# Kernel tuning notes

Hardware: AMD Instinct MI355X
Metric: run time of the kernel (lower is better)

Reference implementation:

```python
import jax, jax.numpy as jnp
import numpy as np

N_NODES = 20000
N_EDGES = 160000
N_GRAPHS = 100
IN_CH = 64
EDGE_DIM = 8
NEG_SLOPE = 0.2


def _gatv2(x, edge_index, edge_attr, Wl, Wr, We, att, b, heads, ch, n_nodes):
    # GATv2Conv: e_ij = att . leaky_relu(Wl x_j + Wr x_i [+ We e_ij]), softmax over dst i,
    # out_i = sum_j alpha_ij * (Wl x_j), concat heads, + bias.
    src, dst = edge_index[0], edge_index[1]
    xl = (x @ Wl).reshape(-1, heads, ch)  # [N,H,C] source-side transform
    xr = (x @ Wr).reshape(-1, heads, ch)  # [N,H,C] target-side transform
    m = xl[src] + xr[dst]                 # [E,H,C]
    if edge_attr is not None:
        m = m + (edge_attr @ We).reshape(-1, heads, ch)
    m = jax.nn.leaky_relu(m, NEG_SLOPE)
    logit = jnp.einsum('ehc,hc->eh', m, att)                     # [E,H]
    mx = jax.ops.segment_max(logit, dst, num_segments=n_nodes)   # [N,H]
    ex = jnp.exp(logit - mx[dst])
    den = jax.ops.segment_sum(ex, dst, num_segments=n_nodes)     # [N,H]
    alpha = ex / (den[dst] + 1e-16)                              # [E,H]
    out = jax.ops.segment_sum(alpha[:, :, None] * xl[src], dst, num_segments=n_nodes)
    return out.reshape(-1, heads * ch) + b


def setup_inputs() -> dict:
    key = jax.random.key(0)
    ks = jax.random.split(key, 24)
    def rn(k, shape, fan_in):
        return jax.random.normal(k, shape, dtype=jnp.float32) / np.sqrt(fan_in)
    inp = {}
    inp['x'] = jax.random.normal(ks[0], (N_NODES, IN_CH), dtype=jnp.float32)
    inp['edge_attr'] = jax.random.uniform(ks[1], (N_EDGES, EDGE_DIM), dtype=jnp.float32)
    inp['Wl1'] = rn(ks[2], (IN_CH, 1024), IN_CH)
    inp['Wr1'] = rn(ks[3], (IN_CH, 1024), IN_CH)
    inp['We1'] = rn(ks[4], (EDGE_DIM, 1024), EDGE_DIM)
    inp['att1'] = rn(ks[5], (4, 256), 256)
    inp['b1'] = jnp.zeros((1024,), jnp.float32)
    inp['Wl2'] = rn(ks[6], (1024, 256), 1024)
    inp['Wr2'] = rn(ks[7], (1024, 256), 1024)
    inp['We2'] = rn(ks[8], (EDGE_DIM, 256), EDGE_DIM)
    inp['att2'] = rn(ks[9], (4, 64), 64)
    inp['b2'] = jnp.zeros((256,), jnp.float32)
    inp['Wlp'] = rn(ks[10], (256, 384), 256)
    inp['Wrp'] = rn(ks[11], (256, 384), 256)
    inp['attp'] = rn(ks[12], (6, 64), 64)
    inp['bp'] = jnp.zeros((384,), jnp.float32)
    inp['Wfc1'] = rn(ks[13], (384, 64), 384)
    inp['bfc1'] = jnp.zeros((64,), jnp.float32)
    inp['Wfc2'] = rn(ks[14], (64, 1), 64)
    inp['bfc2'] = jnp.zeros((1,), jnp.float32)
    inp['edge_index'] = jax.random.randint(ks[15], (2, N_EDGES), 0, N_NODES, dtype=jnp.int32)
    inp['edge_index_master'] = jax.random.randint(ks[16], (2, N_EDGES), 0, N_NODES, dtype=jnp.int32)
    inp['n_nodes'] = jnp.full((N_GRAPHS,), N_NODES // N_GRAPHS, dtype=jnp.int32)
    return inp


def reference(x, edge_attr, Wl1, Wr1, We1, att1, b1, Wl2, Wr2, We2, att2, b2,
              Wlp, Wrp, attp, bp, Wfc1, bfc1, Wfc2, bfc2,
              edge_index, edge_index_master, n_nodes):
    h = _gatv2(x, edge_index, edge_attr, Wl1, Wr1, We1, att1, b1, 4, 256, N_NODES)
    h = jax.nn.relu(h)
    h = _gatv2(h, edge_index, edge_attr, Wl2, Wr2, We2, att2, b2, 4, 64, N_NODES)
    h = jax.nn.relu(h)
    h = _gatv2(h, edge_index_master, None, Wlp, Wrp, None, attp, bp, 6, 64, N_NODES)
    last_idx = jnp.cumsum(n_nodes) - 1          # master node = last node of each graph
    master = h[last_idx]                        # [G,384] (dropout p=0 -> identity)
    z = jax.nn.relu(master @ Wfc1 + bfc1)
    return z @ Wfc2 + bfc2                      # [G,1]
```

## Files before the change

kernel.cpp:

```cpp
#include <hip/hip_runtime.h>
#include <hip/hip_bf16.h>

#define DIV_UP(a,b) (((a)+(b)-1)/(b))

typedef __attribute__((ext_vector_type(8))) short short8;
typedef __attribute__((ext_vector_type(4))) float floatx4;

static __device__ __forceinline__ unsigned short f2bf(float v) {
    unsigned u = __builtin_bit_cast(unsigned, v);
    u += 0x7fffu + ((u >> 16) & 1u);
    return (unsigned short)(u >> 16);
}
static __device__ __forceinline__ float bflo(unsigned v) {
    return __builtin_bit_cast(float, v << 16);
}
static __device__ __forceinline__ float bfhi(unsigned v) {
    return __builtin_bit_cast(float, v & 0xffff0000u);
}

template <int CPL>
static __device__ __forceinline__ void load_bf16v(const unsigned short* p, float* d) {
    if constexpr (CPL == 8) {
        uint4 v = *(const uint4*)p;
        d[0] = bflo(v.x); d[1] = bfhi(v.x);
        d[2] = bflo(v.y); d[3] = bfhi(v.y);
        d[4] = bflo(v.z); d[5] = bfhi(v.z);
        d[6] = bflo(v.w); d[7] = bfhi(v.w);
    } else if constexpr (CPL == 4) {
        uint2 v = *(const uint2*)p;
        d[0] = bflo(v.x); d[1] = bfhi(v.x);
        d[2] = bflo(v.y); d[3] = bfhi(v.y);
    } else if constexpr (CPL == 2) {
        unsigned v = *(const unsigned*)p;
        d[0] = bflo(v); d[1] = bfhi(v);
    } else {
        d[0] = bflo(*p);
    }
}

template <int CPL>
static __device__ __forceinline__ void store_bf16v(unsigned short* p, const float* s) {
    unsigned short tmp[CPL];
#pragma unroll
    for (int c = 0; c < CPL; ++c) tmp[c] = f2bf(s[c]);
    if constexpr (CPL == 8) *(uint4*)p = *(uint4*)tmp;
    else if constexpr (CPL == 4) *(ushort4*)p = *(ushort4*)tmp;
    else if constexpr (CPL == 2) *(ushort2*)p = *(ushort2*)tmp;
    else p[0] = tmp[0];
}

template <int CTRL>
static __device__ __forceinline__ float dpp_mv(float x) {
    int r = __builtin_amdgcn_update_dpp(0, __builtin_bit_cast(int, x), CTRL, 0xF, 0xF, false);
    return __builtin_bit_cast(float, r);
}
template <int G>
static __device__ __forceinline__ float group_reduce(float x) {
    x += dpp_mv<0xB1>(x);
    x += dpp_mv<0x4E>(x);
    x += dpp_mv<0x124>(x);
    x += dpp_mv<0x128>(x);
    if constexpr (G >= 32) x += __shfl_xor(x, 16, 64);
    if constexpr (G >= 64) x += __shfl_xor(x, 32, 64);
    return x;
}

static __device__ __forceinline__ void tr_pair(const float* Wa, const float* Wb, int K, int Nn,
                                               unsigned short* Wt, int i) {
    int tot = K * Nn;
    const float* W = (i < tot) ? Wa : Wb;
    unsigned short* dst = Wt + ((i < tot) ? 0 : (size_t)Nn * K);
    int ii = (i < tot) ? i : i - tot;
    int k = ii % K, n = ii / K;
    dst[(size_t)n * K + k] = f2bf(W[(size_t)k * Nn + n]);
}

__global__ void prep_all(const float* __restrict__ x,
                         const float* __restrict__ Wl1, const float* __restrict__ Wr1,
                         const float* __restrict__ Wl2, const float* __restrict__ Wr2,
                         const float* __restrict__ Wlp, const float* __restrict__ Wrp,
                         unsigned short* __restrict__ xbf,
                         unsigned short* __restrict__ wt1, unsigned short* __restrict__ wt2,
                         unsigned short* __restrict__ wt3, int N) {
    const int S1 = 2 * 64 * 1024, S2 = 2 * 1024 * 256, S3 = 2 * 256 * 384;
    int id = blockIdx.x * blockDim.x + threadIdx.x;
    if (id < S1) tr_pair(Wl1, Wr1, 64, 1024, wt1, id);
    else if (id < S1 + S2) tr_pair(Wl2, Wr2, 1024, 256, wt2, id - S1);
    else if (id < S1 + S2 + S3) tr_pair(Wlp, Wrp, 256, 384, wt3, id - S1 - S2);
    else {
        int i = id - S1 - S2 - S3;
        if (i < N * 64) xbf[i] = f2bf(x[i]);
    }
}

__global__ __launch_bounds__(256) void gemm_mfma(
    const unsigned short* __restrict__ A, const unsigned short* __restrict__ Bt,
    unsigned short* __restrict__ C, int M, int Ntot, int K) {
    constexpr int LDA = 40;
    __shared__ unsigned short As[128 * LDA];
    __shared__ unsigned short Bs[128 * LDA];
    const int tid = threadIdx.x;
    const int m0 = blockIdx.y * 128, n0 = blockIdx.x * 128;
    const int wave = tid >> 6, lane = tid & 63;
    const int wm = (wave >> 1) * 64, wn = (wave & 1) * 64;
    const int r15 = lane & 15, quad = lane >> 4;
    const int sr = tid >> 1, skc = tid & 1;
    floatx4 acc[4][4];
#pragma unroll
    for (int i = 0; i < 4; ++i)
#pragma unroll
        for (int j = 0; j < 4; ++j) acc[i][j] = (floatx4)0.f;

    for (int k0 = 0; k0 < K; k0 += 32) {
        uint4 a0 = make_uint4(0, 0, 0, 0), a1 = make_uint4(0, 0, 0, 0);
        int am = m0 + sr;
        if (am < M) {
            const unsigned short* ap = A + (size_t)am * K + k0 + skc * 16;
            a0 = *(const uint4*)ap;
            a1 = *(const uint4*)(ap + 8);
        }
        const unsigned short* bp = Bt + (size_t)(n0 + sr) * K + k0 + skc * 16;
        uint4 b0 = *(const uint4*)bp;
        uint4 b1 = *(const uint4*)(bp + 8);
        *(uint4*)(&As[sr * LDA + skc * 16]) = a0;
        *(uint4*)(&As[sr * LDA + skc * 16 + 8]) = a1;
        *(uint4*)(&Bs[sr * LDA + skc * 16]) = b0;
        *(uint4*)(&Bs[sr * LDA + skc * 16 + 8]) = b1;
        __syncthreads();
        short8 af[4], bfr[4];
#pragma unroll
        for (int i = 0; i < 4; ++i)
            af[i] = *(const short8*)(&As[(wm + i * 16 + r15) * LDA + quad * 8]);
#pragma unroll
        for (int j = 0; j < 4; ++j)
            bfr[j] = *(const short8*)(&Bs[(wn + j * 16 + r15) * LDA + quad * 8]);
#pragma unroll
        for (int i = 0; i < 4; ++i)
#pragma unroll
            for (int j = 0; j < 4; ++j)
                acc[i][j] = __builtin_amdgcn_mfma_f32_16x16x32_bf16(af[i], bfr[j], acc[i][j], 0, 0, 0);
        __syncthreads();
    }
#pragma unroll
    for (int i = 0; i < 4; ++i)
#pragma unroll
        for (int j = 0; j < 4; ++j)
#pragma unroll
            for (int r = 0; r < 4; ++r) {
                int m = m0 + wm + i * 16 + quad * 4 + r;
                int n = n0 + wn + j * 16 + r15;
                if (m < M) C[(size_t)m * Ntot + n] = f2bf(acc[i][j][r]);
            }
}

__global__ void count2_kernel(const int* __restrict__ dst0, const int* __restrict__ dst1,
                              int E, int N, int* __restrict__ cnt) {
    int e = blockIdx.x * blockDim.x + threadIdx.x;
    if (e < E) atomicAdd(&cnt[dst0[e]], 1);
    else if (e < 2 * E) atomicAdd(&cnt[N + dst1[e - E]], 1);
}

__global__ __launch_bounds__(1024) void scan_kernel(const int* __restrict__ cnt_all, int N,
                                                    int* __restrict__ off_all, int* __restrict__ cur_all) {
    const int* cnt = cnt_all + blockIdx.x * N;
    int* off = off_all + blockIdx.x * (N + 1);
    int* cur = cur_all + blockIdx.x * N;
    __shared__ int part[1024];
    int t = threadIdx.x;
    int per = (N + 1023) >> 10;
    int base = t * per;
    int s = 0;
    for (int i = 0; i < per; ++i) { int idx = base + i; if (idx < N) s += cnt[idx]; }
    part[t] = s;
    __syncthreads();
    for (int d2 = 1; d2 < 1024; d2 <<= 1) {
        int v = (t >= d2) ? part[t - d2] : 0;
        __syncthreads();
        part[t] += v;
        __syncthreads();
    }
    int pre = (t == 0) ? 0 : part[t - 1];
    for (int i = 0; i < per; ++i) {
        int idx = base + i;
        if (idx < N) { off[idx] = pre; cur[idx] = pre; pre += cnt[idx]; }
    }
    if (t == 1023) off[N] = part[1023];
}

__global__ void fill2_kernel(const int* __restrict__ src0, const int* __restrict__ dst0,
                             const int* __restrict__ src1, const int* __restrict__ dst1,
                             int E, int N, int* __restrict__ cur, int2* __restrict__ edges) {
    int e = blockIdx.x * blockDim.x + threadIdx.x;
    if (e < E) {
        int p = atomicAdd(&cur[dst0[e]], 1);
        edges[p] = make_int2(src0[e], e);
    } else if (e < 2 * E) {
        int i = e - E;
        int p = atomicAdd(&cur[N + dst1[i]], 1);
        edges[E + p] = make_int2(src1[i], i);
    }
}

template <int D, int CPL, int QP, int G, int NE>
static __device__ __forceinline__ void hase_group(
    const unsigned short* __restrict__ xlr, const float* __restrict__ ea,
    const float* wb, const float (&att_r)[CPL], const float (&xr_r)[CPL],
    const int2* ep , int c0,
    float& m, float& l, float (&acc)[CPL]) {
    int2 e[NE];
#pragma unroll
    for (int n = 0; n < NE; ++n) e[n] = ep[n];
    float ev[NE][8];
#pragma unroll
    for (int n = 0; n < NE; ++n) {
        float4 a = ((const float4*)(ea + (size_t)e[n].y * 8))[0];
        float4 b = ((const float4*)(ea + (size_t)e[n].y * 8))[1];
        ev[n][0] = a.x; ev[n][1] = a.y; ev[n][2] = a.z; ev[n][3] = a.w;
        ev[n][4] = b.x; ev[n][5] = b.y; ev[n][6] = b.z; ev[n][7] = b.w;
    }
    float xv[NE][CPL], z[NE][CPL];
#pragma unroll
    for (int n = 0; n < NE; ++n) {
        load_bf16v<CPL>(xlr + (size_t)e[n].x * (2 * D) + c0, xv[n]);
#pragma unroll
        for (int c = 0; c < CPL; ++c) z[n][c] = xv[n][c] + xr_r[c];
    }
#pragma unroll
    for (int k = 0; k < 8; ++k) {
#pragma unroll
        for (int q = 0; q < CPL / 4; ++q) {
            float4 w4 = *(const float4*)(wb + k * D + q * QP);
#pragma unroll
            for (int n = 0; n < NE; ++n) {
                z[n][q * 4 + 0] = fmaf(ev[n][k], w4.x, z[n][q * 4 + 0]);
                z[n][q * 4 + 1] = fmaf(ev[n][k], w4.y, z[n][q * 4 + 1]);
                z[n][q * 4 + 2] = fmaf(ev[n][k], w4.z, z[n][q * 4 + 2]);
                z[n][q * 4 + 3] = fmaf(ev[n][k], w4.w, z[n][q * 4 + 3]);
            }
        }
    }
    float lg[NE];
#pragma unroll
    for (int n = 0; n < NE; ++n) {
        lg[n] = 0.f;
#pragma unroll
        for (int c = 0; c < CPL; ++c) {
            float a = z[n][c] > 0.f ? z[n][c] : 0.2f * z[n][c];
            lg[n] = fmaf(att_r[c], a, lg[n]);
        }
        lg[n] = group_reduce<G>(lg[n]);
    }
    float mn = m;
#pragma unroll
    for (int n = 0; n < NE; ++n) mn = fmaxf(mn, lg[n]);
    float sc = __expf(m - mn);
    float p[NE], ps = 0.f;
#pragma unroll
    for (int n = 0; n < NE; ++n) { p[n] = __expf(lg[n] - mn); ps += p[n]; }
    m = mn;
    l = fmaf(l, sc, ps);
#pragma unroll
    for (int c = 0; c < CPL; ++c) {
        float t = p[0] * xv[0][c];
#pragma unroll
        for (int n = 1; n < NE; ++n) t = fmaf(p[n], xv[n][c], t);
        acc[c] = fmaf(acc[c], sc, t);
    }
}

template <int D, int C, int CB, int WPN, bool RELU>
__global__ __launch_bounds__(256) void attn_hase(
    const unsigned short* __restrict__ xlr, const float* __restrict__ ea,
    const float* __restrict__ We, const float* __restrict__ att,
    const int2* __restrict__ edges, const int* __restrict__ off,
    const float* __restrict__ bias, unsigned short* __restrict__ outp, int N) {
    constexpr int CPL = CB / 64;
    constexpr int HW = CB / C;
    constexpr int G = 64 / HW;
    constexpr int NPB = 4 / WPN;
    constexpr int QP = CB * 4 / CPL;
    __shared__ float wsh[8 * D];
    for (int f4 = threadIdx.x; f4 < 2 * D; f4 += 256) {
        int k = f4 / (D / 4);
        int c = (f4 - k * (D / 4)) * 4;
        int b = c / CB, cc = c - b * CB;
        int ln = cc / CPL, q = (cc % CPL) / 4;
        int dst = k * (D / 4) + (b * CB + q * QP + ln * 4) / 4;
        ((float4*)wsh)[dst] = ((const float4*)We)[f4];
    }
    __syncthreads();

    const int wid = threadIdx.x >> 6, lane = threadIdx.x & 63;
    const int wv = wid % WPN, wn = wid / WPN;
    const int c0 = wv * CB + lane * CPL;
    const float* wb = wsh + wv * CB + lane * 4;

    float att_r[CPL];
#pragma unroll
    for (int c = 0; c < CPL; ++c) att_r[c] = att[c0 + c];

    for (int node = blockIdx.x * NPB + wn; node < N; node += gridDim.x * NPB) {
        float xr_r[CPL];
        load_bf16v<CPL>(xlr + (size_t)node * (2 * D) + D + c0, xr_r);
        float m = -1e30f, l = 0.f, acc[CPL];
#pragma unroll
        for (int c = 0; c < CPL; ++c) acc[c] = 0.f;

        const int jb = __builtin_amdgcn_readfirstlane(off[node]);
        const int je = __builtin_amdgcn_readfirstlane(off[node + 1]);
        int j = jb;
        for (; j + 4 <= je; j += 4)
            hase_group<D, CPL, QP, G, 4>(xlr, ea, wb, att_r, xr_r, edges + j, c0, m, l, acc);
        for (; j < je; ++j)
            hase_group<D, CPL, QP, G, 1>(xlr, ea, wb, att_r, xr_r, edges + j, c0, m, l, acc);

        float inv = 1.f / (l + 1e-16f);
        float r[CPL];
#pragma unroll
        for (int c = 0; c < CPL; ++c) {
            r[c] = fmaf(acc[c], inv, bias[c0 + c]);
            if constexpr (RELU) r[c] = fmaxf(r[c], 0.f);
        }
        store_bf16v<CPL>(outp + (size_t)node * D + c0, r);
    }
}

template <int D, int CPL, int G, int NE>
static __device__ __forceinline__ void noe_group(
    const unsigned short* __restrict__ xlr,
    const float (&att_r)[CPL], const float (&xr_r)[CPL],
    const int2* ep , int c0,
    float& m, float& l, float (&acc)[CPL]) {
    int2 e[NE];
#pragma unroll
    for (int n = 0; n < NE; ++n) e[n] = ep[n];
    float xv[NE][CPL], lg[NE];
#pragma unroll
    for (int n = 0; n < NE; ++n)
        load_bf16v<CPL>(xlr + (size_t)e[n].x * (2 * D) + c0, xv[n]);
#pragma unroll
    for (int n = 0; n < NE; ++n) {
        lg[n] = 0.f;
#pragma unroll
        for (int c = 0; c < CPL; ++c) {
            float z = xv[n][c] + xr_r[c];
            z = z > 0.f ? z : 0.2f * z;
            lg[n] = fmaf(att_r[c], z, lg[n]);
        }
        lg[n] = group_reduce<G>(lg[n]);
    }
    float mn = m;
#pragma unroll
    for (int n = 0; n < NE; ++n) mn = fmaxf(mn, lg[n]);
    float sc = __expf(m - mn);
    float p[NE], ps = 0.f;
#pragma unroll
    for (int n = 0; n < NE; ++n) { p[n] = __expf(lg[n] - mn); ps += p[n]; }
    m = mn;
    l = fmaf(l, sc, ps);
#pragma unroll
    for (int c = 0; c < CPL; ++c) {
        float t = p[0] * xv[0][c];
#pragma unroll
        for (int n = 1; n < NE; ++n) t = fmaf(p[n], xv[n][c], t);
        acc[c] = fmaf(acc[c], sc, t);
    }
}

template <int D, int C, int CB, bool RELU>
static __device__ __forceinline__ void attn_wave3(
    const unsigned short* __restrict__ xlr, const float* __restrict__ att,
    const int2* __restrict__ edges, int jb, int je,
    const float* __restrict__ bias, float* __restrict__ outp,
    int node, int cb, int lane) {
    constexpr int CPL = CB / 64;
    constexpr int HW = CB / C;
    constexpr int G = 64 / HW;
    const int c0 = cb + lane * CPL;

    float xr_r[CPL], att_r[CPL];
    load_bf16v<CPL>(xlr + (size_t)node * (2 * D) + D + c0, xr_r);
#pragma unroll
    for (int c = 0; c < CPL; ++c) att_r[c] = att[c0 + c];

    float m = -1e30f, l = 0.f, acc[CPL];
#pragma unroll
    for (int c = 0; c < CPL; ++c) acc[c] = 0.f;

    int j = jb;
    for (; j + 4 <= je; j += 4)
        noe_group<D, CPL, G, 4>(xlr, att_r, xr_r, edges + j, c0, m, l, acc);
    for (; j < je; ++j)
        noe_group<D, CPL, G, 1>(xlr, att_r, xr_r, edges + j, c0, m, l, acc);

    float inv = 1.f / (l + 1e-16f);
    float* out = outp + (size_t)node * D + c0;
    float tmp[CPL];
#pragma unroll
    for (int c = 0; c < CPL; ++c) {
        float r = fmaf(acc[c], inv, bias[c0 + c]);
        if constexpr (RELU) r = fmaxf(r, 0.f);
        tmp[c] = r;
    }
    if constexpr (CPL == 4) *(float4*)out = *(float4*)tmp;
    else if constexpr (CPL == 2) *(float2*)out = *(float2*)tmp;
    else out[0] = tmp[0];
}

template <int D, int C, int CB0, int CB1, bool RELU>
__global__ __launch_bounds__(256) void attn_noe(
    const unsigned short* __restrict__ xlr, const float* __restrict__ att,
    const int2* __restrict__ edges, const int* __restrict__ off,
    const float* __restrict__ bias, float* __restrict__ outp, int N) {
    const int wid = threadIdx.x >> 6, lane = threadIdx.x & 63;
    const int gw = blockIdx.x * 4 + wid;
    const int node = gw >> 1, wv = gw & 1;
    if (node >= N) return;
    const int jb = __builtin_amdgcn_readfirstlane(off[node]);
    const int je = __builtin_amdgcn_readfirstlane(off[node + 1]);
    if (wv == 0)
        attn_wave3<D, C, CB0, RELU>(xlr, att, edges, jb, je, bias, outp, node, 0, lane);
    else
        attn_wave3<D, C, CB1, RELU>(xlr, att, edges, jb, je, bias, outp, node, CB0, lane);
}

__global__ void mlp_kernel(const float* __restrict__ h3, const int* __restrict__ nn,
                           const float* __restrict__ Wfc1, const float* __restrict__ bfc1,
                           const float* __restrict__ Wfc2, const float* __restrict__ bfc2,
                           float* __restrict__ out, int G) {
    int g = blockIdx.x, t = threadIdx.x;
    int s = 0;
    for (int k = 0; k <= g; ++k) s += nn[k];
    const float* row = h3 + (size_t)(s - 1) * 384;
    float z = bfc1[t];
    for (int k = 0; k < 384; ++k) z = fmaf(row[k], Wfc1[k * 64 + t], z);
    z = fmaxf(z, 0.f);
    float v = z * Wfc2[t];
#pragma unroll
    for (int o = 32; o; o >>= 1) v += __shfl_xor(v, o, 64);
    if (t == 0) out[g] = v + bfc2[0];
}

extern "C" void kernel_launch(void* const* d_in, const int* in_sizes, int n_in,
                              void* d_out, int out_size, void* d_ws, size_t ws_size,
                              hipStream_t stream) {
    const float* x    = (const float*)d_in[0];
    const float* ea   = (const float*)d_in[1];
    const float* Wl1  = (const float*)d_in[2];
    const float* Wr1  = (const float*)d_in[3];
    const float* We1  = (const float*)d_in[4];
    const float* att1 = (const float*)d_in[5];
    const float* b1   = (const float*)d_in[6];
    const float* Wl2  = (const float*)d_in[7];
    const float* Wr2  = (const float*)d_in[8];
    const float* We2  = (const float*)d_in[9];
    const float* att2 = (const float*)d_in[10];
    const float* b2   = (const float*)d_in[11];
    const float* Wlp  = (const float*)d_in[12];
    const float* Wrp  = (const float*)d_in[13];
    const float* attp = (const float*)d_in[14];
    const float* bp   = (const float*)d_in[15];
    const float* Wfc1 = (const float*)d_in[16];
    const float* bfc1 = (const float*)d_in[17];
    const float* Wfc2 = (const float*)d_in[18];
    const float* bfc2 = (const float*)d_in[19];
    const int* ei     = (const int*)d_in[20];
    const int* eim    = (const int*)d_in[21];
    const int* nn     = (const int*)d_in[22];

    const int N = in_sizes[0] / 64;
    const int E = in_sizes[20] / 2;
    const int G = in_sizes[22];
    const int* src1 = ei,  *dst1 = ei + E;
    const int* srcm = eim, *dstm = eim + E;

    char* w = (char*)d_ws;
    size_t o = 0;
    auto alloc = [&](size_t b) { size_t r = o; o += (b + 255) & ~(size_t)255; return r; };
    char* R1 = w + alloc((size_t)N * 2048 * 2);
    unsigned short* xlr1 = (unsigned short*)R1;
    unsigned short* xlr3 = (unsigned short*)R1;
    float* h3 = (float*)(R1 + (size_t)N * 768 * 2 + 256);
    unsigned short* h1   = (unsigned short*)(w + alloc((size_t)N * 1024 * 2));
    unsigned short* xlr2 = (unsigned short*)(w + alloc((size_t)N * 512 * 2));
    unsigned short* h2   = (unsigned short*)(w + alloc((size_t)N * 256 * 2));
    unsigned short* xbf  = (unsigned short*)(w + alloc((size_t)N * 64 * 2));
    unsigned short* wt1  = (unsigned short*)(w + alloc((size_t)2048 * 64 * 2));
    unsigned short* wt2  = (unsigned short*)(w + alloc((size_t)512 * 1024 * 2));
    unsigned short* wt3  = (unsigned short*)(w + alloc((size_t)768 * 256 * 2));
    int*  cnt   = (int*)(w + alloc((size_t)2 * N * 4));
    int*  off   = (int*)(w + alloc((size_t)2 * (N + 1) * 4));
    int*  cur   = (int*)(w + alloc((size_t)2 * N * 4));
    int2* edges = (int2*)(w + alloc((size_t)2 * E * 8 + 4096));
    (void)ws_size; (void)n_in; (void)out_size;

    dim3 blk(256);

    {
        int tot = 2 * 64 * 1024 + 2 * 1024 * 256 + 2 * 256 * 384 + N * 64;
        prep_all<<<DIV_UP(tot, 256), blk, 0, stream>>>(x, Wl1, Wr1, Wl2, Wr2, Wlp, Wrp,
                                                       xbf, wt1, wt2, wt3, N);
    }

    hipMemsetAsync(cnt, 0, (size_t)2 * N * 4, stream);
    count2_kernel<<<DIV_UP(2 * E, 256), blk, 0, stream>>>(dst1, dstm, E, N, cnt);
    scan_kernel<<<2, 1024, 0, stream>>>(cnt, N, off, cur);
    fill2_kernel<<<DIV_UP(2 * E, 256), blk, 0, stream>>>(src1, dst1, srcm, dstm, E, N, cur, edges);
    const int* off3 = off + (N + 1);
    int2* edges3 = edges + E;

    gemm_mfma<<<dim3(2048 / 128, DIV_UP(N, 128)), blk, 0, stream>>>(xbf, wt1, xlr1, N, 2048, 64);
    attn_hase<1024, 256, 512, 2, true><<<2560, blk, 0, stream>>>(
        xlr1, ea, We1, att1, edges, off, b1, h1, N);

    gemm_mfma<<<dim3(512 / 128, DIV_UP(N, 128)), blk, 0, stream>>>(h1, wt2, xlr2, N, 512, 1024);
    attn_hase<256, 64, 256, 1, true><<<1280, blk, 0, stream>>>(
        xlr2, ea, We2, att2, edges, off, b2, h2, N);

    gemm_mfma<<<dim3(768 / 128, DIV_UP(N, 128)), blk, 0, stream>>>(h2, wt3, xlr3, N, 768, 256);
    attn_noe<384, 64, 256, 128, false><<<DIV_UP(N, 2), blk, 0, stream>>>(
        xlr3, attp, edges3, off3, bp, h3, N);

    mlp_kernel<<<G, 64, 0, stream>>>(h3, nn, Wfc1, bfc1, Wfc2, bfc2, (float*)d_out, G);
}
```

Before: 422.8 us.

## Pack attention math into v_pk_fma and pre-gather edge attrs in CSR order

Rewrites the edge attention inner loops to use packed float2 ops (v_pk_fma_f32, packed leaky relu) and folds log2(e) into the attention vector so exp2 replaces expf. Adds a dup_ea kernel that gathers edge attributes into CSR order, duplicated per pair, so the attention kernel reads them contiguously instead of gathering by edge id. The duplicated buffers reuse the xlr2 and h1 scratch regions, which depends on those buffers not being live at the time. The price is two extra small kernels and twice the edge-attribute bytes.

```diff
diff --git a/kernel.cpp b/kernel.cpp
--- a/kernel.cpp
+++ b/kernel.cpp
@@ -5,6 +5,7 @@
 
 typedef __attribute__((ext_vector_type(8))) short short8;
 typedef __attribute__((ext_vector_type(4))) float floatx4;
+typedef __attribute__((ext_vector_type(2))) float float2v;
 
 static __device__ __forceinline__ unsigned short f2bf(float v) {
     unsigned u = __builtin_bit_cast(unsigned, v);
@@ -18,23 +19,34 @@
     return __builtin_bit_cast(float, v & 0xffff0000u);
 }
 
+static __device__ __forceinline__ float2v mk2(float a, float b) {
+    float2v r; r[0] = a; r[1] = b; return r;
+}
+static __device__ __forceinline__ float2v pk_fma(float2v a, float2v b, float2v c) {
+    float2v d;
+    asm("v_pk_fma_f32 %0, %1, %2, %3" : "=v"(d) : "v"(a), "v"(b), "v"(c));
+    return d;
+}
+static __device__ __forceinline__ float2v pk_leaky(float2v z) {
+    return __builtin_elementwise_max(z, z * 0.2f);
+}
+static __device__ __forceinline__ float fexp2(float x) { return __builtin_amdgcn_exp2f(x); }
+
 template <int CPL>
-static __device__ __forceinline__ void load_bf16v(const unsigned short* p, float* d) {
+static __device__ __forceinline__ void load_bf16p(const unsigned short* p, float2v* d) {
     if constexpr (CPL == 8) {
         uint4 v = *(const uint4*)p;
-        d[0] = bflo(v.x); d[1] = bfhi(v.x);
-        d[2] = bflo(v.y); d[3] = bfhi(v.y);
-        d[4] = bflo(v.z); d[5] = bfhi(v.z);
-        d[6] = bflo(v.w); d[7] = bfhi(v.w);
+        d[0] = mk2(bflo(v.x), bfhi(v.x));
+        d[1] = mk2(bflo(v.y), bfhi(v.y));
+        d[2] = mk2(bflo(v.z), bfhi(v.z));
+        d[3] = mk2(bflo(v.w), bfhi(v.w));
     } else if constexpr (CPL == 4) {
         uint2 v = *(const uint2*)p;
-        d[0] = bflo(v.x); d[1] = bfhi(v.x);
-        d[2] = bflo(v.y); d[3] = bfhi(v.y);
-    } else if constexpr (CPL == 2) {
+        d[0] = mk2(bflo(v.x), bfhi(v.x));
+        d[1] = mk2(bflo(v.y), bfhi(v.y));
+    } else {
         unsigned v = *(const unsigned*)p;
-        d[0] = bflo(v); d[1] = bfhi(v);
-    } else {
-        d[0] = bflo(*p);
+        d[0] = mk2(bflo(v), bfhi(v));
     }
 }
 
@@ -201,80 +213,102 @@
     }
 }
 
+__global__ void dup_ea_kernel(const float* __restrict__ ea, const int2* __restrict__ edges,
+                              float* __restrict__ ead, int E) {
+    int j = blockIdx.x * blockDim.x + threadIdx.x;
+    if (j >= E) return;
+    int ey = edges[j].y;
+    float4 a = ((const float4*)(ea + (size_t)ey * 8))[0];
+    float4 b = ((const float4*)(ea + (size_t)ey * 8))[1];
+    float4* o = (float4*)(ead + (size_t)j * 16);
+    o[0] = make_float4(a.x, a.x, a.y, a.y);
+    o[1] = make_float4(a.z, a.z, a.w, a.w);
+    o[2] = make_float4(b.x, b.x, b.y, b.y);
+    o[3] = make_float4(b.z, b.z, b.w, b.w);
+}
+
 template <int D, int CPL, int QP, int G, int NE>
 static __device__ __forceinline__ void hase_group(
-    const unsigned short* __restrict__ xlr, const float* __restrict__ ea,
-    const float* wb, const float (&att_r)[CPL], const float (&xr_r)[CPL],
+    const unsigned short* __restrict__ xlr, const float* __restrict__ ej,
+    const float* wb, const float2v (&att2)[CPL / 2], const float2v (&xr2)[CPL / 2],
     const int2* ep , int c0,
-    float& m, float& l, float (&acc)[CPL]) {
+    float& m, float& l, float2v (&acc2)[CPL / 2]) {
+    constexpr int P = CPL / 2;
     int2 e[NE];
 #pragma unroll
     for (int n = 0; n < NE; ++n) e[n] = ep[n];
-    float ev[NE][8];
+
+    float2v xv2[NE][P], z2[NE][P];
 #pragma unroll
     for (int n = 0; n < NE; ++n) {
-        float4 a = ((const float4*)(ea + (size_t)e[n].y * 8))[0];
-        float4 b = ((const float4*)(ea + (size_t)e[n].y * 8))[1];
-        ev[n][0] = a.x; ev[n][1] = a.y; ev[n][2] = a.z; ev[n][3] = a.w;
-        ev[n][4] = b.x; ev[n][5] = b.y; ev[n][6] = b.z; ev[n][7] = b.w;
-    }
-    float xv[NE][CPL], z[NE][CPL];
-#pragma unroll
-    for (int n = 0; n < NE; ++n) {
-        load_bf16v<CPL>(xlr + (size_t)e[n].x * (2 * D) + c0, xv[n]);
-#pragma unroll
-        for (int c = 0; c < CPL; ++c) z[n][c] = xv[n][c] + xr_r[c];
-    }
-#pragma unroll
-    for (int k = 0; k < 8; ++k) {
-#pragma unroll
-        for (int q = 0; q < CPL / 4; ++q) {
-            float4 w4 = *(const float4*)(wb + k * D + q * QP);
-#pragma unroll
-            for (int n = 0; n < NE; ++n) {
-                z[n][q * 4 + 0] = fmaf(ev[n][k], w4.x, z[n][q * 4 + 0]);
-                z[n][q * 4 + 1] = fmaf(ev[n][k], w4.y, z[n][q * 4 + 1]);
-                z[n][q * 4 + 2] = fmaf(ev[n][k], w4.z, z[n][q * 4 + 2]);
-                z[n][q * 4 + 3] = fmaf(ev[n][k], w4.w, z[n][q * 4 + 3]);
+        load_bf16p<CPL>(xlr + (size_t)e[n].x * (2 * D) + c0, xv2[n]);
+#pragma unroll
+        for (int p = 0; p < P; ++p) z2[n][p] = xv2[n][p] + xr2[p];
+    }
+#pragma unroll
+    for (int h = 0; h < 2; ++h) {
+        float2v ev[NE][4];
+#pragma unroll
+        for (int n = 0; n < NE; ++n) {
+            const float4* q = (const float4*)(ej + (size_t)n * 16 + h * 8);
+            float4 t0 = q[0], t1 = q[1];
+            ev[n][0] = mk2(t0.x, t0.y); ev[n][1] = mk2(t0.z, t0.w);
+            ev[n][2] = mk2(t1.x, t1.y); ev[n][3] = mk2(t1.z, t1.w);
+        }
+#pragma unroll
+        for (int kk = 0; kk < 4; ++kk) {
+            int k = h * 4 + kk;
+#pragma unroll
+            for (int q = 0; q < CPL / 4; ++q) {
+                float4 w4 = *(const float4*)(wb + k * D + q * QP);
+                float2v wa = mk2(w4.x, w4.y), wc = mk2(w4.z, w4.w);
+#pragma unroll
+                for (int n = 0; n < NE; ++n) {
+                    z2[n][2 * q]     = pk_fma(ev[n][kk], wa, z2[n][2 * q]);
+                    z2[n][2 * q + 1] = pk_fma(ev[n][kk], wc, z2[n][2 * q + 1]);
+                }
             }
         }
     }
     float lg[NE];
 #pragma unroll
     for (int n = 0; n < NE; ++n) {
-        lg[n] = 0.f;
-#pragma unroll
-        for (int c = 0; c < CPL; ++c) {
-            float a = z[n][c] > 0.f ? z[n][c] : 0.2f * z[n][c];
-            lg[n] = fmaf(att_r[c], a, lg[n]);
-        }
-        lg[n] = group_reduce<G>(lg[n]);
+        float2v s = mk2(0.f, 0.f);
+#pragma unroll
+        for (int p = 0; p < P; ++p)
+            s = pk_fma(att2[p], pk_leaky(z2[n][p]), s);
+        lg[n] = group_reduce<G>(s[0] + s[1]);
     }
     float mn = m;
 #pragma unroll
     for (int n = 0; n < NE; ++n) mn = fmaxf(mn, lg[n]);
-    float sc = __expf(m - mn);
-    float p[NE], ps = 0.f;
-#pragma unroll
-    for (int n = 0; n < NE; ++n) { p[n] = __expf(lg[n] - mn); ps += p[n]; }
+    float sc = fexp2(m - mn);
+    float pr[NE], ps = 0.f;
+#pragma unroll
+    for (int n = 0; n < NE; ++n) { pr[n] = fexp2(lg[n] - mn); ps += pr[n]; }
     m = mn;
     l = fmaf(l, sc, ps);
-#pragma unroll
-    for (int c = 0; c < CPL; ++c) {
-        float t = p[0] * xv[0][c];
-#pragma unroll
-        for (int n = 1; n < NE; ++n) t = fmaf(p[n], xv[n][c], t);
-        acc[c] = fmaf(acc[c], sc, t);
+    float2v scp = mk2(sc, sc);
+    float2v prp[NE];
+#pragma unroll
+    for (int n = 0; n < NE; ++n) prp[n] = mk2(pr[n], pr[n]);
+#pragma unroll
+    for (int p = 0; p < P; ++p) {
+        float2v t = prp[0] * xv2[0][p];
+#pragma unroll
+        for (int n = 1; n < NE; ++n) t = pk_fma(prp[n], xv2[n][p], t);
+        acc2[p] = pk_fma(acc2[p], scp, t);
     }
 }
 
 template <int D, int C, int CB, int WPN, bool RELU>
 __global__ __launch_bounds__(256) void attn_hase(
-    const unsigned short* __restrict__ xlr, const float* __restrict__ ea,
+    const unsigned short* __restrict__ xlr, const float* __restrict__ ead,
     const float* __restrict__ We, const float* __restrict__ att,
     const int2* __restrict__ edges, const int* __restrict__ off,
     const float* __restrict__ bias, unsigned short* __restrict__ outp, int N) {
     constexpr int CPL = CB / 64;
+    constexpr int P = CPL / 2;
     constexpr int HW = CB / C;
     constexpr int G = 64 / HW;
     constexpr int NPB = 4 / WPN;
@@ -295,31 +329,40 @@
     const int c0 = wv * CB + lane * CPL;
     const float* wb = wsh + wv * CB + lane * 4;
 
-    float att_r[CPL];
-#pragma unroll
-    for (int c = 0; c < CPL; ++c) att_r[c] = att[c0 + c];
+    const float L2E = 1.4426950408889634f;
+    float2v att2[P];
+#pragma unroll
+    for (int p = 0; p < P; ++p)
+        att2[p] = mk2(att[c0 + 2 * p] * L2E, att[c0 + 2 * p + 1] * L2E);
 
     for (int node = blockIdx.x * NPB + wn; node < N; node += gridDim.x * NPB) {
-        float xr_r[CPL];
-        load_bf16v<CPL>(xlr + (size_t)node * (2 * D) + D + c0, xr_r);
-        float m = -1e30f, l = 0.f, acc[CPL];
-#pragma unroll
-        for (int c = 0; c < CPL; ++c) acc[c] = 0.f;
+        float2v xr2[P];
+        load_bf16p<CPL>(xlr + (size_t)node * (2 * D) + D + c0, xr2);
+        float m = -1e30f, l = 0.f;
+        float2v acc2[P];
+#pragma unroll
+        for (int p = 0; p < P; ++p) acc2[p] = mk2(0.f, 0.f);
 
         const int jb = __builtin_amdgcn_readfirstlane(off[node]);
         const int je = __builtin_amdgcn_readfirstlane(off[node + 1]);
         int j = jb;
         for (; j + 4 <= je; j += 4)
-            hase_group<D, CPL, QP, G, 4>(xlr, ea, wb, att_r, xr_r, edges + j, c0, m, l, acc);
+            hase_group<D, CPL, QP, G, 4>(xlr, ead + (size_t)j * 16, wb, att2, xr2,
+                                         edges + j, c0, m, l, acc2);
         for (; j < je; ++j)
-            hase_group<D, CPL, QP, G, 1>(xlr, ea, wb, att_r, xr_r, edges + j, c0, m, l, acc);
+            hase_group<D, CPL, QP, G, 1>(xlr, ead + (size_t)j * 16, wb, att2, xr2,
+                                         edges + j, c0, m, l, acc2);
 
         float inv = 1.f / (l + 1e-16f);
         float r[CPL];
 #pragma unroll
-        for (int c = 0; c < CPL; ++c) {
-            r[c] = fmaf(acc[c], inv, bias[c0 + c]);
-            if constexpr (RELU) r[c] = fmaxf(r[c], 0.f);
+        for (int p = 0; p < P; ++p) {
+            r[2 * p]     = fmaf(acc2[p][0], inv, bias[c0 + 2 * p]);
+            r[2 * p + 1] = fmaf(acc2[p][1], inv, bias[c0 + 2 * p + 1]);
+        }
+        if constexpr (RELU) {
+#pragma unroll
+            for (int c = 0; c < CPL; ++c) r[c] = fmaxf(r[c], 0.f);
         }
         store_bf16v<CPL>(outp + (size_t)node * D + c0, r);
     }
@@ -328,42 +371,47 @@
 template <int D, int CPL, int G, int NE>
 static __device__ __forceinline__ void noe_group(
     const unsigned short* __restrict__ xlr,
-    const float (&att_r)[CPL], const float (&xr_r)[CPL],
+    const float2v (&att2)[CPL / 2], const float2v (&xr2)[CPL / 2],
     const int2* ep , int c0,
-    float& m, float& l, float (&acc)[CPL]) {
+    float& m, float& l, float2v (&acc2)[CPL / 2]) {
+    constexpr int P = CPL / 2;
     int2 e[NE];
 #pragma unroll
     for (int n = 0; n < NE; ++n) e[n] = ep[n];
-    float xv[NE][CPL], lg[NE];
+    float2v xv2[NE][P];
+    float lg[NE];
 #pragma unroll
     for (int n = 0; n < NE; ++n)
-        load_bf16v<CPL>(xlr + (size_t)e[n].x * (2 * D) + c0, xv[n]);
+        load_bf16p<CPL>(xlr + (size_t)e[n].x * (2 * D) + c0, xv2[n]);
 #pragma unroll
     for (int n = 0; n < NE; ++n) {
-        lg[n] = 0.f;
-#pragma unroll
-        for (int c = 0; c < CPL; ++c) {
-            float z = xv[n][c] + xr_r[c];
-            z = z > 0.f ? z : 0.2f * z;
-            lg[n] = fmaf(att_r[c], z, lg[n]);
+        float2v s = mk2(0.f, 0.f);
+#pragma unroll
+        for (int p = 0; p < P; ++p) {
+            float2v z = xv2[n][p] + xr2[p];
+            s = pk_fma(att2[p], pk_leaky(z), s);
         }
-        lg[n] = group_reduce<G>(lg[n]);
+        lg[n] = group_reduce<G>(s[0] + s[1]);
     }
     float mn = m;
 #pragma unroll
     for (int n = 0; n < NE; ++n) mn = fmaxf(mn, lg[n]);
-    float sc = __expf(m - mn);
-    float p[NE], ps = 0.f;
-#pragma unroll
-    for (int n = 0; n < NE; ++n) { p[n] = __expf(lg[n] - mn); ps += p[n]; }
+    float sc = fexp2(m - mn);
+    float pr[NE], ps = 0.f;
+#pragma unroll
+    for (int n = 0; n < NE; ++n) { pr[n] = fexp2(lg[n] - mn); ps += pr[n]; }
     m = mn;
     l = fmaf(l, sc, ps);
-#pragma unroll
-    for (int c = 0; c < CPL; ++c) {
-        float t = p[0] * xv[0][c];
-#pragma unroll
-        for (int n = 1; n < NE; ++n) t = fmaf(p[n], xv[n][c], t);
-        acc[c] = fmaf(acc[c], sc, t);
+    float2v scp = mk2(sc, sc);
+    float2v prp[NE];
+#pragma unroll
+    for (int n = 0; n < NE; ++n) prp[n] = mk2(pr[n], pr[n]);
+#pragma unroll
+    for (int p = 0; p < P; ++p) {
+        float2v t = prp[0] * xv2[0][p];
+#pragma unroll
+        for (int n = 1; n < NE; ++n) t = pk_fma(prp[n], xv2[n][p], t);
+        acc2[p] = pk_fma(acc2[p], scp, t);
     }
 }
 
@@ -374,33 +422,38 @@
     const float* __restrict__ bias, float* __restrict__ outp,
     int node, int cb, int lane) {
     constexpr int CPL = CB / 64;
+    constexpr int P = CPL / 2;
     constexpr int HW = CB / C;
     constexpr int G = 64 / HW;
     const int c0 = cb + lane * CPL;
-
-    float xr_r[CPL], att_r[CPL];
-    load_bf16v<CPL>(xlr + (size_t)node * (2 * D) + D + c0, xr_r);
-#pragma unroll
-    for (int c = 0; c < CPL; ++c) att_r[c] = att[c0 + c];
-
-    float m = -1e30f, l = 0.f, acc[CPL];
-#pragma unroll
-    for (int c = 0; c < CPL; ++c) acc[c] = 0.f;
+    const float L2E = 1.4426950408889634f;
+
+    float2v xr2[P], att2[P];
+    load_bf16p<CPL>(xlr + (size_t)node * (2 * D) + D + c0, xr2);
+#pragma unroll
+    for (int p = 0; p < P; ++p)
+        att2[p] = mk2(att[c0 + 2 * p] * L2E, att[c0 + 2 * p + 1] * L2E);
+
+    float m = -1e30f, l = 0.f;
+    float2v acc2[P];
+#pragma unroll
+    for (int p = 0; p < P; ++p) acc2[p] = mk2(0.f, 0.f);
 
     int j = jb;
     for (; j + 4 <= je; j += 4)
-        noe_group<D, CPL, G, 4>(xlr, att_r, xr_r, edges + j, c0, m, l, acc);
+        noe_group<D, CPL, G, 4>(xlr, att2, xr2, edges + j, c0, m, l, acc2);
     for (; j < je; ++j)
-        noe_group<D, CPL, G, 1>(xlr, att_r, xr_r, edges + j, c0, m, l, acc);
+        noe_group<D, CPL, G, 1>(xlr, att2, xr2, edges + j, c0, m, l, acc2);
 
     float inv = 1.f / (l + 1e-16f);
     float* out = outp + (size_t)node * D + c0;
     float tmp[CPL];
 #pragma unroll
-    for (int c = 0; c < CPL; ++c) {
-        float r = fmaf(acc[c], inv, bias[c0 + c]);
-        if constexpr (RELU) r = fmaxf(r, 0.f);
-        tmp[c] = r;
+    for (int p = 0; p < P; ++p) {
+        float r0 = fmaf(acc2[p][0], inv, bias[c0 + 2 * p]);
+        float r1 = fmaf(acc2[p][1], inv, bias[c0 + 2 * p + 1]);
+        if constexpr (RELU) { r0 = fmaxf(r0, 0.f); r1 = fmaxf(r1, 0.f); }
+        tmp[2 * p] = r0; tmp[2 * p + 1] = r1;
     }
     if constexpr (CPL == 4) *(float4*)out = *(float4*)tmp;
     else if constexpr (CPL == 2) *(float2*)out = *(float2*)tmp;
@@ -494,6 +547,9 @@
     int2* edges = (int2*)(w + alloc((size_t)2 * E * 8 + 4096));
     (void)ws_size; (void)n_in; (void)out_size;
 
+    float* ead1 = (float*)xlr2;
+    float* ead2 = (float*)h1;
+
     dim3 blk(256);
 
     {
@@ -506,16 +562,18 @@
     count2_kernel<<<DIV_UP(2 * E, 256), blk, 0, stream>>>(dst1, dstm, E, N, cnt);
     scan_kernel<<<2, 1024, 0, stream>>>(cnt, N, off, cur);
     fill2_kernel<<<DIV_UP(2 * E, 256), blk, 0, stream>>>(src1, dst1, srcm, dstm, E, N, cur, edges);
+    dup_ea_kernel<<<DIV_UP(E, 256), blk, 0, stream>>>(ea, edges, ead1, E);
     const int* off3 = off + (N + 1);
     int2* edges3 = edges + E;
 
     gemm_mfma<<<dim3(2048 / 128, DIV_UP(N, 128)), blk, 0, stream>>>(xbf, wt1, xlr1, N, 2048, 64);
     attn_hase<1024, 256, 512, 2, true><<<2560, blk, 0, stream>>>(
-        xlr1, ea, We1, att1, edges, off, b1, h1, N);
+        xlr1, ead1, We1, att1, edges, off, b1, h1, N);
 
     gemm_mfma<<<dim3(512 / 128, DIV_UP(N, 128)), blk, 0, stream>>>(h1, wt2, xlr2, N, 512, 1024);
+    dup_ea_kernel<<<DIV_UP(E, 256), blk, 0, stream>>>(ea, edges, ead2, E);
     attn_hase<256, 64, 256, 1, true><<<1280, blk, 0, stream>>>(
-        xlr2, ea, We2, att2, edges, off, b2, h2, N);
+        xlr2, ead2, We2, att2, edges, off, b2, h2, N);
 
     gemm_mfma<<<dim3(768 / 128, DIV_UP(N, 128)), blk, 0, stream>>>(h2, wt3, xlr3, N, 768, 256);
     attn_noe<384, 64, 256, 128, false><<<DIV_UP(N, 2), blk, 0, stream>>>(
```

Measured after the change: 440.1 us. 4.1% more time.
